# Kernel tuning notes

Measured on AMD Instinct MI355X. Metric: run time of the kernel, lower is better.

The kernel has to match this reference:

```python
import jax, jax.numpy as jnp
import numpy as np

N_GRAPHS = 512
NODES_PER_G = 200
EDGES_PER_G = 6400
N = N_GRAPHS * NODES_PER_G        # 102400 nodes
E = N_GRAPHS * EDGES_PER_G        # 3276800 edges
HID = 128
NCLS = 10


def _linear_params(key, fan_in, fan_out):
    # torch nn.Linear default init: U(-1/sqrt(fan_in), 1/sqrt(fan_in))
    s = 1.0 / np.sqrt(fan_in)
    kw, kb = jax.random.split(key)
    W = jax.random.uniform(kw, (fan_in, fan_out), minval=-s, maxval=s, dtype=jnp.float32)
    b = jax.random.uniform(kb, (fan_out,), minval=-s, maxval=s, dtype=jnp.float32)
    return W, b


def setup_inputs() -> dict:
    key = jax.random.key(0)
    ks = jax.random.split(key, 10)
    # edges are confined within each graph (DGL batched graph structure)
    g_off = (jnp.arange(E, dtype=jnp.int32) // EDGES_PER_G) * NODES_PER_G
    src = (g_off + jax.random.randint(ks[0], (E,), 0, NODES_PER_G)).astype(jnp.int32)
    dst = (g_off + jax.random.randint(ks[1], (E,), 0, NODES_PER_G)).astype(jnp.int32)
    W1, b1 = _linear_params(ks[2], 1, HID)
    W2, b2 = _linear_params(ks[3], HID, HID)
    Wa, ba = _linear_params(ks[4], HID, 512)
    Wb, bb = _linear_params(ks[5], 512, 1024)
    Wc, bc = _linear_params(ks[6], 1024, 1024)
    Wd, bd = _linear_params(ks[7], 1024, 512)
    We, be = _linear_params(ks[8], 512, NCLS)
    return dict(src=src, dst=dst, W1=W1, b1=b1, W2=W2, b2=b2,
                Wa=Wa, ba=ba, Wb=Wb, bb=bb, Wc=Wc, bc=bc,
                Wd=Wd, bd=bd, We=We, be=be)


def reference(src, dst, W1, b1, W2, b2, Wa, ba, Wb, bb, Wc, bc, Wd, bd, We, be):
    seg = jax.ops.segment_sum
    ones = jnp.ones((E,), jnp.float32)
    in_deg = seg(ones, dst, num_segments=N)    # [N]
    out_deg = seg(ones, src, num_segments=N)   # [N]
    # DGL GraphConv norm='both': degrees clamped to min 1
    inv_out = (1.0 / jnp.sqrt(jnp.maximum(out_deg, 1.0)))[:, None]
    inv_in = (1.0 / jnp.sqrt(jnp.maximum(in_deg, 1.0)))[:, None]

    def gconv(h, W, b):
        h = (h @ W) * inv_out                    # src-side normalize (weight applied first; same math)
        h = seg(h[src], dst, num_segments=N)     # gather + scatter-add aggregation
        return h * inv_in + b                    # dst-side normalize + bias

    h = in_deg[:, None]                          # input node features = in-degrees, [N,1]
    h = jax.nn.relu(gconv(h, W1, b1))
    h = jax.nn.relu(gconv(h, W2, b2))

    gid = jnp.arange(N, dtype=jnp.int32) // NODES_PER_G
    hg = seg(h, gid, num_segments=N_GRAPHS) / float(NODES_PER_G)  # mean readout, [G,HID]

    x = jax.nn.relu(hg @ Wa + ba)
    x = jax.nn.relu(x @ Wb + bb)
    x = jax.nn.relu(x @ Wc + bc)
    x = jax.nn.relu(x @ Wd + bd)
    return jax.nn.softmax(x @ We + be, axis=-1)  # nn.Softmax over class dim
```

## Files before the change

kernel.cpp:

```cpp
#include <hip/hip_runtime.h>
#include <stdint.h>

typedef unsigned short u16;
typedef unsigned int   u32;

#define NG   512
#define NPG  200
#define EPG  6400
#define NN   (NG*NPG)
#define NE_  (NG*EPG)
#define HID  128
#define KP   224
#define AW   224
#define AG   57344
#define ZP   136

__device__ __forceinline__ float bf2f(u16 b){ u32 u = ((u32)b) << 16; return __builtin_bit_cast(float, u); }
__device__ __forceinline__ u16 f2bf(float f){
    u32 u = __builtin_bit_cast(u32, f);
    u = (u + 0x7FFFu + ((u >> 16) & 1u)) >> 16;
    return (u16)u;
}

typedef __attribute__((ext_vector_type(8))) short bf16x8;
typedef __attribute__((ext_vector_type(4))) float f32x4;

enum : int { cW1=0, cb1=128, cb2=256, cba=384, cbb=896, cbc=1920, cbd=2944, cWe=3456, cbe=8576, cEND=8586 };
enum : int { T_Wa=0, T_Wb=65536, T_Wc=589824, T_Wd=1638400, T_END=2162688 };
enum : int { B0=8586, B1=24970, B2=2187658 };

struct PrepIn { const void* p[14]; };

__global__ __launch_bounds__(256) void k_prep(PrepIn in, float* __restrict__ canon,
                                              u16* __restrict__ W2T, u16* __restrict__ WTa)
{
    __shared__ int sflag;
    const int tid = threadIdx.x;
    if (tid < 64){
        const u16* wb = (const u16*)in.p[0];
        u16 a = wb[tid], b = wb[64 + tid];
        unsigned long long m1 = __ballot((int)((a >> 7) & 0xFF) >= 0x7F);
        unsigned long long m2 = __ballot((int)((b >> 7) & 0xFF) >= 0x7F);
        if (tid == 0) sflag = (__popcll(m1) + __popcll(m2) > 4) ? 1 : 0;
    }
    __syncthreads();
    const int f = sflag;

    int i = blockIdx.x * 256 + tid;
    if (i >= B2) return;

    if (i < B0){
        const void* s; int off;
        if      (i < 128) { s = in.p[0];  off = i; }
        else if (i < 256) { s = in.p[1];  off = i - 128; }
        else if (i < 384) { s = in.p[3];  off = i - 256; }
        else if (i < 896) { s = in.p[5];  off = i - 384; }
        else if (i < 1920){ s = in.p[7];  off = i - 896; }
        else if (i < 2944){ s = in.p[9];  off = i - 1920; }
        else if (i < 3456){ s = in.p[11]; off = i - 2944; }
        else if (i < 8576){ s = in.p[12]; off = i - 3456; }
        else              { s = in.p[13]; off = i - 8576; }
        canon[i] = f ? ((const float*)s)[off] : bf2f(((const u16*)s)[off]);
    } else if (i < B1){
        int j = i - B0;
        int outc = j >> 7, inc = j & 127;
        int si = inc * HID + outc;
        W2T[j] = f ? f2bf(((const float*)in.p[2])[si]) : ((const u16*)in.p[2])[si];
    } else {
        int j = i - B1;
        const void* s; int si;
        if (j < T_Wb){ s = in.p[4];  int n = j >> 7,  k = j & 127;  si = k*512  + n; }
        else if (j < T_Wc){ int jj = j - T_Wb; s = in.p[6];  int n = jj >> 9,  k = jj & 511;  si = k*1024 + n; }
        else if (j < T_Wd){ int jj = j - T_Wc; s = in.p[8];  int n = jj >> 10, k = jj & 1023; si = k*1024 + n; }
        else              { int jj = j - T_Wd; s = in.p[10]; int n = jj >> 10, k = jj & 1023; si = k*512  + n; }
        WTa[j] = f ? f2bf(((const float*)s)[si]) : ((const u16*)s)[si];
    }
}

__global__ __launch_bounds__(512) void k_graph_prep(
    const int* __restrict__ src, const int* __restrict__ dst,
    const float* __restrict__ W1, const float* __restrict__ b1,
    float* __restrict__ invInG, u16* __restrict__ h1sT,
    u16* __restrict__ Adense)
{
    __shared__ u32 A32[AG/2];
    __shared__ u16 srcL[EPG];
    __shared__ u16 dstL[EPG];
    __shared__ int degIn[NPG];
    __shared__ int degOut[NPG];
    __shared__ float sValL[NPG], sAgg[NPG], iiL[NPG], ioL[NPG], tL[NPG];
    __shared__ float w1L[HID], b1L[HID];

    const int g = blockIdx.x, tid = threadIdx.x;

    uint4* a4 = (uint4*)A32;
    #pragma unroll
    for (int i = 0; i < AG/8/512; i++)
        a4[i*512 + tid] = make_uint4(0,0,0,0);
    if (tid < NPG){ degIn[tid] = 0; degOut[tid] = 0; sAgg[tid] = 0.f; }
    if (tid < HID){ w1L[tid] = W1[tid]; b1L[tid] = b1[tid]; }
    __syncthreads();

    const int ebase = g * EPG;
    #pragma unroll
    for (int i = 0; i < (EPG + 511)/512; i++){
        int e = i*512 + tid;
        if (e < EPG){
            int s = src[ebase + e] - g*NPG;
            int d = dst[ebase + e] - g*NPG;
            srcL[e] = (u16)s; dstL[e] = (u16)d;
            atomicAdd(&degOut[s], 1);
            atomicAdd(&degIn[d], 1);
        }
    }
    __syncthreads();

    if (tid < NPG){
        int din = degIn[tid], dout = degOut[tid];
        float ii = rsqrtf(fmaxf((float)din, 1.f));
        float io = rsqrtf(fmaxf((float)dout, 1.f));
        iiL[tid] = ii; ioL[tid] = io;
        sValL[tid] = (float)din * io;
        invInG[g*NPG + tid] = ii;
    }
    __syncthreads();

    #pragma unroll
    for (int i = 0; i < (EPG + 511)/512; i++){
        int e = i*512 + tid;
        if (e < EPG){
            int s = srcL[e], d = dstL[e];
            int q = (d * 41) >> 11;
            int idx = (q*64 + (d - q*50))*AW + s;
            atomicAdd(&A32[idx >> 1], 1u << (16*(idx & 1)));
            atomicAdd(&sAgg[d], sValL[s]);
        }
    }
    __syncthreads();

    if (tid < NPG) tL[tid] = sAgg[tid] * iiL[tid];
    __syncthreads();

    const size_t base = (size_t)g * HID * KP;
    #pragma unroll 4
    for (int i = 0; i < HID*KP/512; i++){
        int idx = i*512 + tid;
        int c = idx / KP, v = idx - c*KP;
        u16 o = 0;
        if (v < NPG)
            o = f2bf(fmaxf(fmaf(tL[v], w1L[c], b1L[c]), 0.f) * ioL[v]);
        h1sT[base + idx] = o;
    }

    uint4* g4 = (uint4*)(Adense + (size_t)g * AG);
    #pragma unroll 4
    for (int i = 0; i < AG/8/512; i++){
        uint4 v = a4[i*512 + tid];
        u32* pv = (u32*)&v;
        #pragma unroll
        for (int j = 0; j < 4; j++){
            u32 wv = pv[j];
            pv[j] = (u32)f2bf((float)(wv & 0xFFFFu)) | ((u32)f2bf((float)(wv >> 16)) << 16);
        }
        g4[i*512 + tid] = v;
    }
}

__global__ __launch_bounds__(512, 4) void k_fused_graph(
    const u16* __restrict__ Adense,
    const u16* __restrict__ h1sT, const u16* __restrict__ W2T,
    const float* __restrict__ invInG, const float* __restrict__ b2,
    float* __restrict__ hg)
{
    __shared__ __align__(16) u16 Zs[256*ZP];
    __shared__ float invInL[256];
    __shared__ float b2L[HID];
    __shared__ float poolL[HID];

    const int g = blockIdx.x, tid = threadIdx.x;

    if (tid < HID){ b2L[tid] = b2[tid]; poolL[tid] = 0.f; }
    if (tid < 256){
        int dl = tid & 63;
        invInL[tid] = (dl < 50) ? invInG[g*NPG + (tid >> 6)*50 + dl] : 0.f;
    }

    const int w = tid >> 6, lane = tid & 63;
    const int wm = w >> 2, wn = w & 3;
    const int lr = lane & 15, quad = lane >> 4;

    const f32x4 fz = {0.f, 0.f, 0.f, 0.f};

    f32x4 acc[4][4];
    #pragma unroll
    for (int mi = 0; mi < 4; mi++)
        #pragma unroll
        for (int nt = 0; nt < 4; nt++) acc[mi][nt] = fz;
    {
        const u16* Ap = h1sT + (size_t)g * HID * KP + (size_t)(wm*64) * KP;
        const u16* Bp = Adense + (size_t)g * AG + (size_t)(wn*64) * AW;
        for (int ks = 0; ks < 7; ks++){
            bf16x8 af[4], bf[4];
            #pragma unroll
            for (int mi = 0; mi < 4; mi++)
                af[mi] = *(const bf16x8*)&Ap[(mi*16 + lr)*KP + ks*32 + quad*8];
            #pragma unroll
            for (int nt = 0; nt < 4; nt++)
                bf[nt] = *(const bf16x8*)&Bp[(nt*16 + lr)*AW + ks*32 + quad*8];
            #pragma unroll
            for (int mi = 0; mi < 4; mi++)
                #pragma unroll
                for (int nt = 0; nt < 4; nt++)
                    acc[mi][nt] = __builtin_amdgcn_mfma_f32_16x16x32_bf16(
                        af[mi], bf[nt], acc[mi][nt], 0, 0, 0);
        }
    }

    #pragma unroll
    for (int mi = 0; mi < 4; mi++)
        #pragma unroll
        for (int nt = 0; nt < 4; nt++){
            int vq = wn*64 + nt*16 + lr;
            int c0 = wm*64 + mi*16 + quad*4;
            u16 z0 = f2bf(acc[mi][nt][0]), z1 = f2bf(acc[mi][nt][1]);
            u16 z2 = f2bf(acc[mi][nt][2]), z3 = f2bf(acc[mi][nt][3]);
            uint2 pk = { (u32)z0 | ((u32)z1 << 16), (u32)z2 | ((u32)z3 << 16) };
            *(uint2*)&Zs[vq*ZP + c0] = pk;
        }
    __syncthreads();

    f32x4 acc2[2][8];
    #pragma unroll
    for (int mi = 0; mi < 2; mi++)
        #pragma unroll
        for (int nt = 0; nt < 8; nt++) acc2[mi][nt] = fz;
    for (int ks = 0; ks < 4; ks++){
        bf16x8 za[2];
        #pragma unroll
        for (int mi = 0; mi < 2; mi++)
            za[mi] = *(const bf16x8*)&Zs[((w + mi*8)*16 + lr)*ZP + ks*32 + quad*8];
        #pragma unroll
        for (int nt = 0; nt < 8; nt++){
            bf16x8 wb = *(const bf16x8*)&W2T[(size_t)(nt*16 + lr)*HID + ks*32 + quad*8];
            #pragma unroll
            for (int mi = 0; mi < 2; mi++)
                acc2[mi][nt] = __builtin_amdgcn_mfma_f32_16x16x32_bf16(
                    za[mi], wb, acc2[mi][nt], 0, 0, 0);
        }
    }

    #pragma unroll
    for (int mi = 0; mi < 2; mi++)
        #pragma unroll
        for (int nt = 0; nt < 8; nt++){
            int cout = nt*16 + lr;
            float s = 0.f;
            #pragma unroll
            for (int r = 0; r < 4; r++){
                int vq = (w + mi*8)*16 + quad*4 + r;
                if ((vq & 63) < 50)
                    s += fmaxf(fmaf(acc2[mi][nt][r], invInL[vq], b2L[cout]), 0.f);
            }
            atomicAdd(&poolL[cout], s);
        }
    __syncthreads();
    if (tid < HID) hg[(size_t)g*HID + tid] = poolL[tid] * (1.f / NPG);
}

template<int K, bool AF32>
__global__ __launch_bounds__(512) void k_mlp5(
    const void* __restrict__ Ahi_, const u16* __restrict__ Alo,
    const u16* __restrict__ WT, const float* __restrict__ bias,
    u16* __restrict__ Ohi, u16* __restrict__ Olo, int Nc)
{
    constexpr int ITERS = K / 64;
    __shared__ __align__(16) float red[32][68];

    const int tid = threadIdx.x;
    const int w = tid >> 6, lane = tid & 63;
    const int kz = w >> 2, wm = (w >> 1) & 1, wn = w & 1;
    const int lr = lane & 15, quad = lane >> 4;
    const int row0 = blockIdx.x * 32, col0 = blockIdx.y * 64;
    const int m = row0 + wm*16 + lr;
    const int k0 = kz * (K/2);

    const float* Af = (const float*)Ahi_;
    const u16*   Ah = (const u16*)Ahi_;

    auto loadA = [&](int it, bf16x8& hi, bf16x8& lo){
        const int kk = k0 + it*32 + quad*8;
        if constexpr (AF32){
            float xs[8];
            *(float4*)&xs[0] = *(const float4*)&Af[(size_t)m*K + kk];
            *(float4*)&xs[4] = *(const float4*)&Af[(size_t)m*K + kk + 4];
            #pragma unroll
            for (int j = 0; j < 8; j++){
                u16 hh = f2bf(xs[j]);
                hi[j] = (short)hh;
                lo[j] = (short)f2bf(xs[j] - bf2f(hh));
            }
        } else {
            hi = *(const bf16x8*)&Ah[(size_t)m*K + kk];
            lo = *(const bf16x8*)&Alo[(size_t)m*K + kk];
        }
    };
    auto loadB = [&](int it, bf16x8* b){
        const int kk = k0 + it*32 + quad*8;
        #pragma unroll
        for (int nt = 0; nt < 2; nt++){
            int n = col0 + wn*32 + nt*16 + lr;
            b[nt] = *(const bf16x8*)&WT[(size_t)n*K + kk];
        }
    };

    const f32x4 fz = {0.f, 0.f, 0.f, 0.f};
    f32x4 acc[2] = {fz, fz};
    bf16x8 chi, clo, cb[2], nhi, nlo, nb[2];
    loadA(0, chi, clo); loadB(0, cb);
    #pragma unroll 2
    for (int it = 0; it < ITERS; it++){
        if (it + 1 < ITERS){ loadA(it+1, nhi, nlo); loadB(it+1, nb); }
        #pragma unroll
        for (int nt = 0; nt < 2; nt++){
            acc[nt] = __builtin_amdgcn_mfma_f32_16x16x32_bf16(chi, cb[nt], acc[nt], 0, 0, 0);
            acc[nt] = __builtin_amdgcn_mfma_f32_16x16x32_bf16(clo, cb[nt], acc[nt], 0, 0, 0);
        }
        chi = nhi; clo = nlo; cb[0] = nb[0]; cb[1] = nb[1];
    }

    if (kz == 1){
        #pragma unroll
        for (int nt = 0; nt < 2; nt++)
            #pragma unroll
            for (int r = 0; r < 4; r++)
                red[wm*16 + quad*4 + r][wn*32 + nt*16 + lr] = acc[nt][r];
    }
    __syncthreads();
    if (kz == 0){
        #pragma unroll
        for (int nt = 0; nt < 2; nt++)
            #pragma unroll
            for (int r = 0; r < 4; r++){
                int rr = wm*16 + quad*4 + r;
                int cc = wn*32 + nt*16 + lr;
                float v = acc[nt][r] + red[rr][cc] + bias[col0 + cc];
                v = fmaxf(v, 0.f);
                u16 hh = f2bf(v);
                size_t go = (size_t)(row0 + rr) * Nc + col0 + cc;
                Ohi[go] = hh;
                Olo[go] = f2bf(v - bf2f(hh));
            }
    }
}

__global__ __launch_bounds__(64) void k_head(
    const u16* __restrict__ Xhi, const u16* __restrict__ Xlo,
    const float* __restrict__ We, const float* __restrict__ be,
    void* __restrict__ out, const u16* __restrict__ w1bits)
{
    const int g = blockIdx.x, lane = threadIdx.x;
    u16 a = w1bits[lane], b = w1bits[64 + lane];
    unsigned long long m1 = __ballot((int)((a >> 7) & 0xFF) >= 0x7F);
    unsigned long long m2 = __ballot((int)((b >> 7) & 0xFF) >= 0x7F);
    const int f = (__popcll(m1) + __popcll(m2) > 4) ? 1 : 0;

    float part[10];
    #pragma unroll
    for (int c = 0; c < 10; c++) part[c] = 0.f;
    for (int k = lane; k < 512; k += 64){
        float x = bf2f(Xhi[(size_t)g*512 + k]) + bf2f(Xlo[(size_t)g*512 + k]);
        #pragma unroll
        for (int c = 0; c < 10; c++) part[c] = fmaf(x, We[k*10 + c], part[c]);
    }
    #pragma unroll
    for (int c = 0; c < 10; c++){
        float v = part[c];
        for (int off = 32; off > 0; off >>= 1) v += __shfl_down(v, off);
        part[c] = v;
    }
    if (lane == 0){
        #pragma unroll
        for (int c = 0; c < 10; c++) part[c] += be[c];
        float m = part[0];
        #pragma unroll
        for (int c = 1; c < 10; c++) m = fmaxf(m, part[c]);
        float e[10], s = 0.f;
        #pragma unroll
        for (int c = 0; c < 10; c++){ e[c] = __expf(part[c] - m); s += e[c]; }
        float inv = 1.f / s;
        #pragma unroll
        for (int c = 0; c < 10; c++){
            float p = e[c] * inv;
            if (f) ((float*)out)[g*10 + c] = p;
            else   ((u16*)out)[g*10 + c]  = f2bf(p);
        }
    }
}

extern "C" void kernel_launch(void* const* d_in, const int* in_sizes, int n_in,
                              void* d_out, int out_size, void* d_ws, size_t ws_size,
                              hipStream_t stream)
{
    const int* src = (const int*)d_in[0];
    const int* dst = (const int*)d_in[1];

    char* ws = (char*)d_ws;
    size_t o = 0;
    float* canon    = (float*)(ws + o); o += ((size_t)cEND * 4 + 15) & ~(size_t)15;
    u16*   W2T      = (u16*)  (ws + o); o += (size_t)HID * HID * 2;
    u16*   WTa      = (u16*)  (ws + o); o += ((size_t)T_END * 2 + 15) & ~(size_t)15;
    float* invIn    = (float*)(ws + o); o += (size_t)NN * 4;
    u16*   Adense   = (u16*)  (ws + o); o += (size_t)NG * AG * 2;
    u16*   h1sT     = (u16*)  (ws + o); o += (size_t)NG * HID * KP * 2;
    float* hg       = (float*)(ws + o); o += (size_t)NG * HID * 4;
    u16*   X1hi     = (u16*)  (ws + o); o += (size_t)NG * 512 * 2;
    u16*   X1lo     = (u16*)  (ws + o); o += (size_t)NG * 512 * 2;
    u16*   X2hi     = (u16*)  (ws + o); o += (size_t)NG * 1024 * 2;
    u16*   X2lo     = (u16*)  (ws + o); o += (size_t)NG * 1024 * 2;
    u16*   X3hi     = (u16*)  (ws + o); o += (size_t)NG * 1024 * 2;
    u16*   X3lo     = (u16*)  (ws + o); o += (size_t)NG * 1024 * 2;
    u16*   X4hi     = (u16*)  (ws + o); o += (size_t)NG * 512 * 2;
    u16*   X4lo     = (u16*)  (ws + o); o += (size_t)NG * 512 * 2;
    (void)ws_size; (void)in_sizes; (void)n_in; (void)out_size;

    PrepIn pin;
    for (int i = 0; i < 14; i++) pin.p[i] = d_in[2 + i];
    k_prep<<<dim3((B2 + 255)/256), dim3(256), 0, stream>>>(pin, canon, W2T, WTa);

    const float *W1 = canon+cW1, *b1 = canon+cb1, *b2 = canon+cb2;
    const float *ba = canon+cba, *bb = canon+cbb, *bc = canon+cbc, *bd = canon+cbd;
    const float *We = canon+cWe, *be = canon+cbe;

    k_graph_prep<<<dim3(NG), dim3(512), 0, stream>>>(
        src, dst, W1, b1, invIn, h1sT, Adense);

    k_fused_graph<<<dim3(NG), dim3(512), 0, stream>>>(
        Adense, h1sT, W2T, invIn, b2, hg);

    k_mlp5<128,  true ><<<dim3(16, 8),  dim3(512), 0, stream>>>(hg,   nullptr, WTa + T_Wa, ba, X1hi, X1lo, 512);
    k_mlp5<512,  false><<<dim3(16, 16), dim3(512), 0, stream>>>(X1hi, X1lo,    WTa + T_Wb, bb, X2hi, X2lo, 1024);
    k_mlp5<1024, false><<<dim3(16, 16), dim3(512), 0, stream>>>(X2hi, X2lo,    WTa + T_Wc, bc, X3hi, X3lo, 1024);
    k_mlp5<1024, false><<<dim3(16, 8),  dim3(512), 0, stream>>>(X3hi, X3lo,    WTa + T_Wd, bd, X4hi, X4lo, 512);

    k_head<<<dim3(NG), dim3(64), 0, stream>>>(X4hi, X4lo, We, be, d_out, (const u16*)d_in[2]);
}
```

Measured before the change: 279.9 us.

## Fuse graph prep and GCN aggregation into one LDS-resident kernel, tile weight transposes

Merges the graph-preparation and fused-graph kernels into a single per-graph kernel. It keeps the edge list, h1 features and a quarter of the dense adjacency in shared memory and processes destination nodes in four 50-row chunks, so the dense adjacency and h1 intermediates are never written to or read back from global memory. The weight-prep kernel now transposes through a 64x64 shared-memory tile so both reads and writes are coalesced. The trade-off is heavier shared-memory use per block, which lowers occupancy, plus four extra passes over the edge list with more barriers.

```diff
diff --git a/kernel.cpp b/kernel.cpp
--- a/kernel.cpp
+++ b/kernel.cpp
@@ -10,9 +10,7 @@
 #define NN   (NG*NPG)
 #define NE_  (NG*EPG)
 #define HID  128
-#define KP   224
-#define AW   224
-#define AG   57344
+#define HS   232
 #define ZP   136
 
 __device__ __forceinline__ float bf2f(u16 b){ u32 u = ((u32)b) << 16; return __builtin_bit_cast(float, u); }
@@ -27,13 +25,13 @@
 
 enum : int { cW1=0, cb1=128, cb2=256, cba=384, cbb=896, cbc=1920, cbd=2944, cWe=3456, cbe=8576, cEND=8586 };
 enum : int { T_Wa=0, T_Wb=65536, T_Wc=589824, T_Wd=1638400, T_END=2162688 };
-enum : int { B0=8586, B1=24970, B2=2187658 };
 
 struct PrepIn { const void* p[14]; };
 
-__global__ __launch_bounds__(256) void k_prep(PrepIn in, float* __restrict__ canon,
-                                              u16* __restrict__ W2T, u16* __restrict__ WTa)
+__global__ __launch_bounds__(256) void k_prep2(PrepIn in, float* __restrict__ canon,
+                                               u16* __restrict__ W2T, u16* __restrict__ WTa)
 {
+    __shared__ u16 tile[64][72];
     __shared__ int sflag;
     const int tid = threadIdx.x;
     if (tid < 64){
@@ -45,60 +43,67 @@
     }
     __syncthreads();
     const int f = sflag;
-
-    int i = blockIdx.x * 256 + tid;
-    if (i >= B2) return;
-
-    if (i < B0){
-        const void* s; int off;
-        if      (i < 128) { s = in.p[0];  off = i; }
-        else if (i < 256) { s = in.p[1];  off = i - 128; }
-        else if (i < 384) { s = in.p[3];  off = i - 256; }
-        else if (i < 896) { s = in.p[5];  off = i - 384; }
-        else if (i < 1920){ s = in.p[7];  off = i - 896; }
-        else if (i < 2944){ s = in.p[9];  off = i - 1920; }
-        else if (i < 3456){ s = in.p[11]; off = i - 2944; }
-        else if (i < 8576){ s = in.p[12]; off = i - 3456; }
-        else              { s = in.p[13]; off = i - 8576; }
-        canon[i] = f ? ((const float*)s)[off] : bf2f(((const u16*)s)[off]);
-    } else if (i < B1){
-        int j = i - B0;
-        int outc = j >> 7, inc = j & 127;
-        int si = inc * HID + outc;
-        W2T[j] = f ? f2bf(((const float*)in.p[2])[si]) : ((const u16*)in.p[2])[si];
+    const int bid = blockIdx.x;
+
+    if (bid < 532){
+        const void* s; u16* dst; int K, N, t, lgn;
+        if      (bid < 4)  { t = bid;       s = in.p[2];  dst = W2T;        K = 128;  N = 128;  lgn = 1; }
+        else if (bid < 20) { t = bid - 4;   s = in.p[4];  dst = WTa + T_Wa; K = 128;  N = 512;  lgn = 3; }
+        else if (bid < 148){ t = bid - 20;  s = in.p[6];  dst = WTa + T_Wb; K = 512;  N = 1024; lgn = 4; }
+        else if (bid < 404){ t = bid - 148; s = in.p[8];  dst = WTa + T_Wc; K = 1024; N = 1024; lgn = 4; }
+        else               { t = bid - 404; s = in.p[10]; dst = WTa + T_Wd; K = 1024; N = 512;  lgn = 3; }
+        const int k0 = (t >> lgn) * 64, n0 = (t & ((1 << lgn) - 1)) * 64;
+        #pragma unroll
+        for (int i = 0; i < 16; i++){
+            int idx = i*256 + tid;
+            int kk = idx >> 6, nn = idx & 63;
+            int si = (k0 + kk)*N + n0 + nn;
+            tile[nn][kk] = f ? f2bf(((const float*)s)[si]) : ((const u16*)s)[si];
+        }
+        __syncthreads();
+        #pragma unroll
+        for (int i = 0; i < 16; i++){
+            int idx = i*256 + tid;
+            int nn = idx >> 6, kk = idx & 63;
+            dst[(size_t)(n0 + nn)*K + k0 + kk] = tile[nn][kk];
+        }
     } else {
-        int j = i - B1;
-        const void* s; int si;
-        if (j < T_Wb){ s = in.p[4];  int n = j >> 7,  k = j & 127;  si = k*512  + n; }
-        else if (j < T_Wc){ int jj = j - T_Wb; s = in.p[6];  int n = jj >> 9,  k = jj & 511;  si = k*1024 + n; }
-        else if (j < T_Wd){ int jj = j - T_Wc; s = in.p[8];  int n = jj >> 10, k = jj & 1023; si = k*1024 + n; }
-        else              { int jj = j - T_Wd; s = in.p[10]; int n = jj >> 10, k = jj & 1023; si = k*512  + n; }
-        WTa[j] = f ? f2bf(((const float*)s)[si]) : ((const u16*)s)[si];
-    }
-}
-
-__global__ __launch_bounds__(512) void k_graph_prep(
+        int i = (bid - 532)*256 + tid;
+        if (i < cEND){
+            const void* s; int off;
+            if      (i < 128) { s = in.p[0];  off = i; }
+            else if (i < 256) { s = in.p[1];  off = i - 128; }
+            else if (i < 384) { s = in.p[3];  off = i - 256; }
+            else if (i < 896) { s = in.p[5];  off = i - 384; }
+            else if (i < 1920){ s = in.p[7];  off = i - 896; }
+            else if (i < 2944){ s = in.p[9];  off = i - 1920; }
+            else if (i < 3456){ s = in.p[11]; off = i - 2944; }
+            else if (i < 8576){ s = in.p[12]; off = i - 3456; }
+            else              { s = in.p[13]; off = i - 8576; }
+            canon[i] = f ? ((const float*)s)[off] : bf2f(((const u16*)s)[off]);
+        }
+    }
+}
+
+__global__ __launch_bounds__(512) void k_mega(
     const int* __restrict__ src, const int* __restrict__ dst,
     const float* __restrict__ W1, const float* __restrict__ b1,
-    float* __restrict__ invInG, u16* __restrict__ h1sT,
-    u16* __restrict__ Adense)
+    const float* __restrict__ b2, const u16* __restrict__ W2T,
+    float* __restrict__ hg)
 {
-    __shared__ u32 A32[AG/2];
-    __shared__ u16 srcL[EPG];
-    __shared__ u16 dstL[EPG];
-    __shared__ int degIn[NPG];
-    __shared__ int degOut[NPG];
-    __shared__ float sValL[NPG], sAgg[NPG], iiL[NPG], ioL[NPG], tL[NPG];
-    __shared__ float w1L[HID], b1L[HID];
+    __shared__ u32 pkE[EPG];
+    __shared__ __align__(16) u16 h1s[HID*HS];
+    __shared__ __align__(16) u16 Aq[64*HS];
+    __shared__ __align__(16) u16 Zq[64*ZP];
+    __shared__ int degIn[NPG], degOut[NPG];
+    __shared__ float sVal[NPG], sAgg[NPG], iiL[NPG], ioL[NPG], tL[NPG];
+    __shared__ float w1L[HID], b1L[HID], b2L[HID], poolL[HID];
 
     const int g = blockIdx.x, tid = threadIdx.x;
-
-    uint4* a4 = (uint4*)A32;
-    #pragma unroll
-    for (int i = 0; i < AG/8/512; i++)
-        a4[i*512 + tid] = make_uint4(0,0,0,0);
+    u32* aq32 = (u32*)Aq;
+
     if (tid < NPG){ degIn[tid] = 0; degOut[tid] = 0; sAgg[tid] = 0.f; }
-    if (tid < HID){ w1L[tid] = W1[tid]; b1L[tid] = b1[tid]; }
+    if (tid < HID){ w1L[tid] = W1[tid]; b1L[tid] = b1[tid]; b2L[tid] = b2[tid]; poolL[tid] = 0.f; }
     __syncthreads();
 
     const int ebase = g * EPG;
@@ -108,7 +113,7 @@
         if (e < EPG){
             int s = src[ebase + e] - g*NPG;
             int d = dst[ebase + e] - g*NPG;
-            srcL[e] = (u16)s; dstL[e] = (u16)d;
+            pkE[e] = (u32)s | ((u32)d << 16);
             atomicAdd(&degOut[s], 1);
             atomicAdd(&degIn[d], 1);
         }
@@ -116,12 +121,10 @@
     __syncthreads();
 
     if (tid < NPG){
-        int din = degIn[tid], dout = degOut[tid];
-        float ii = rsqrtf(fmaxf((float)din, 1.f));
-        float io = rsqrtf(fmaxf((float)dout, 1.f));
+        float ii = rsqrtf(fmaxf((float)degIn[tid], 1.f));
+        float io = rsqrtf(fmaxf((float)degOut[tid], 1.f));
         iiL[tid] = ii; ioL[tid] = io;
-        sValL[tid] = (float)din * io;
-        invInG[g*NPG + tid] = ii;
+        sVal[tid] = (float)degIn[tid] * io;
     }
     __syncthreads();
 
@@ -129,141 +132,126 @@
     for (int i = 0; i < (EPG + 511)/512; i++){
         int e = i*512 + tid;
         if (e < EPG){
-            int s = srcL[e], d = dstL[e];
-            int q = (d * 41) >> 11;
-            int idx = (q*64 + (d - q*50))*AW + s;
-            atomicAdd(&A32[idx >> 1], 1u << (16*(idx & 1)));
-            atomicAdd(&sAgg[d], sValL[s]);
-        }
-    }
-    __syncthreads();
-
+            u32 u = pkE[e];
+            atomicAdd(&sAgg[u >> 16], sVal[u & 0xFFFF]);
+        }
+    }
+    __syncthreads();
     if (tid < NPG) tL[tid] = sAgg[tid] * iiL[tid];
     __syncthreads();
 
-    const size_t base = (size_t)g * HID * KP;
     #pragma unroll 4
-    for (int i = 0; i < HID*KP/512; i++){
+    for (int i = 0; i < HID*HS/512; i++){
         int idx = i*512 + tid;
-        int c = idx / KP, v = idx - c*KP;
+        int c = idx / HS, v = idx - c*HS;
         u16 o = 0;
         if (v < NPG)
             o = f2bf(fmaxf(fmaf(tL[v], w1L[c], b1L[c]), 0.f) * ioL[v]);
-        h1sT[base + idx] = o;
-    }
-
-    uint4* g4 = (uint4*)(Adense + (size_t)g * AG);
-    #pragma unroll 4
-    for (int i = 0; i < AG/8/512; i++){
-        uint4 v = a4[i*512 + tid];
-        u32* pv = (u32*)&v;
-        #pragma unroll
-        for (int j = 0; j < 4; j++){
-            u32 wv = pv[j];
-            pv[j] = (u32)f2bf((float)(wv & 0xFFFFu)) | ((u32)f2bf((float)(wv >> 16)) << 16);
-        }
-        g4[i*512 + tid] = v;
-    }
-}
-
-__global__ __launch_bounds__(512, 4) void k_fused_graph(
-    const u16* __restrict__ Adense,
-    const u16* __restrict__ h1sT, const u16* __restrict__ W2T,
-    const float* __restrict__ invInG, const float* __restrict__ b2,
-    float* __restrict__ hg)
-{
-    __shared__ __align__(16) u16 Zs[256*ZP];
-    __shared__ float invInL[256];
-    __shared__ float b2L[HID];
-    __shared__ float poolL[HID];
-
-    const int g = blockIdx.x, tid = threadIdx.x;
-
-    if (tid < HID){ b2L[tid] = b2[tid]; poolL[tid] = 0.f; }
-    if (tid < 256){
-        int dl = tid & 63;
-        invInL[tid] = (dl < 50) ? invInG[g*NPG + (tid >> 6)*50 + dl] : 0.f;
-    }
+        h1s[idx] = o;
+    }
+    __syncthreads();
 
     const int w = tid >> 6, lane = tid & 63;
-    const int wm = w >> 2, wn = w & 3;
     const int lr = lane & 15, quad = lane >> 4;
-
     const f32x4 fz = {0.f, 0.f, 0.f, 0.f};
 
-    f32x4 acc[4][4];
-    #pragma unroll
-    for (int mi = 0; mi < 4; mi++)
-        #pragma unroll
-        for (int nt = 0; nt < 4; nt++) acc[mi][nt] = fz;
-    {
-        const u16* Ap = h1sT + (size_t)g * HID * KP + (size_t)(wm*64) * KP;
-        const u16* Bp = Adense + (size_t)g * AG + (size_t)(wn*64) * AW;
+    for (int q = 0; q < 4; q++){
+        uint4* a4 = (uint4*)Aq;
+        for (int i = tid; i < 64*HS/8; i += 512) a4[i] = make_uint4(0,0,0,0);
+        __syncthreads();
+        #pragma unroll
+        for (int i = 0; i < (EPG + 511)/512; i++){
+            int e = i*512 + tid;
+            if (e < EPG){
+                u32 u = pkE[e];
+                int s = u & 0xFFFF, d = u >> 16;
+                int qe = (d * 41) >> 11;
+                if (qe == q){
+                    int idx = (d - q*50)*HS + s;
+                    atomicAdd(&aq32[idx >> 1], 1u << (16*(idx & 1)));
+                }
+            }
+        }
+        __syncthreads();
+        for (int i = tid; i < 64*HS/2; i += 512){
+            u32 wv = aq32[i];
+            if (wv)
+                aq32[i] = (u32)f2bf((float)(wv & 0xFFFFu)) | ((u32)f2bf((float)(wv >> 16)) << 16);
+        }
+        __syncthreads();
+
+        const int wm = w >> 1, wn = w & 1;
+        f32x4 acc[2][2];
+        #pragma unroll
+        for (int mi = 0; mi < 2; mi++)
+            #pragma unroll
+            for (int nt = 0; nt < 2; nt++) acc[mi][nt] = fz;
         for (int ks = 0; ks < 7; ks++){
-            bf16x8 af[4], bf[4];
-            #pragma unroll
-            for (int mi = 0; mi < 4; mi++)
-                af[mi] = *(const bf16x8*)&Ap[(mi*16 + lr)*KP + ks*32 + quad*8];
-            #pragma unroll
-            for (int nt = 0; nt < 4; nt++)
-                bf[nt] = *(const bf16x8*)&Bp[(nt*16 + lr)*AW + ks*32 + quad*8];
-            #pragma unroll
-            for (int mi = 0; mi < 4; mi++)
+            bf16x8 af[2], bf[2];
+            #pragma unroll
+            for (int mi = 0; mi < 2; mi++)
+                af[mi] = *(const bf16x8*)&h1s[(wm*32 + mi*16 + lr)*HS + ks*32 + quad*8];
+            #pragma unroll
+            for (int nt = 0; nt < 2; nt++)
+                bf[nt] = *(const bf16x8*)&Aq[(wn*32 + nt*16 + lr)*HS + ks*32 + quad*8];
+            #pragma unroll
+            for (int mi = 0; mi < 2; mi++)
                 #pragma unroll
-                for (int nt = 0; nt < 4; nt++)
+                for (int nt = 0; nt < 2; nt++)
                     acc[mi][nt] = __builtin_amdgcn_mfma_f32_16x16x32_bf16(
                         af[mi], bf[nt], acc[mi][nt], 0, 0, 0);
         }
-    }
-
-    #pragma unroll
-    for (int mi = 0; mi < 4; mi++)
-        #pragma unroll
-        for (int nt = 0; nt < 4; nt++){
-            int vq = wn*64 + nt*16 + lr;
-            int c0 = wm*64 + mi*16 + quad*4;
-            u16 z0 = f2bf(acc[mi][nt][0]), z1 = f2bf(acc[mi][nt][1]);
-            u16 z2 = f2bf(acc[mi][nt][2]), z3 = f2bf(acc[mi][nt][3]);
-            uint2 pk = { (u32)z0 | ((u32)z1 << 16), (u32)z2 | ((u32)z3 << 16) };
-            *(uint2*)&Zs[vq*ZP + c0] = pk;
-        }
-    __syncthreads();
-
-    f32x4 acc2[2][8];
-    #pragma unroll
-    for (int mi = 0; mi < 2; mi++)
-        #pragma unroll
-        for (int nt = 0; nt < 8; nt++) acc2[mi][nt] = fz;
-    for (int ks = 0; ks < 4; ks++){
-        bf16x8 za[2];
         #pragma unroll
         for (int mi = 0; mi < 2; mi++)
-            za[mi] = *(const bf16x8*)&Zs[((w + mi*8)*16 + lr)*ZP + ks*32 + quad*8];
-        #pragma unroll
-        for (int nt = 0; nt < 8; nt++){
-            bf16x8 wb = *(const bf16x8*)&W2T[(size_t)(nt*16 + lr)*HID + ks*32 + quad*8];
+            #pragma unroll
+            for (int nt = 0; nt < 2; nt++){
+                int vq = wn*32 + nt*16 + lr;
+                int c0 = wm*32 + mi*16 + quad*4;
+                u16 z0 = f2bf(acc[mi][nt][0]), z1 = f2bf(acc[mi][nt][1]);
+                u16 z2 = f2bf(acc[mi][nt][2]), z3 = f2bf(acc[mi][nt][3]);
+                uint2 pk = { (u32)z0 | ((u32)z1 << 16), (u32)z2 | ((u32)z3 << 16) };
+                *(uint2*)&Zq[vq*ZP + c0] = pk;
+            }
+        __syncthreads();
+
+        const int wm2 = w >> 2, wn2 = w & 3;
+        f32x4 acc2[2][2];
+        #pragma unroll
+        for (int mi = 0; mi < 2; mi++)
+            #pragma unroll
+            for (int nt = 0; nt < 2; nt++) acc2[mi][nt] = fz;
+        for (int ks = 0; ks < 4; ks++){
+            bf16x8 za[2], wb[2];
             #pragma unroll
             for (int mi = 0; mi < 2; mi++)
-                acc2[mi][nt] = __builtin_amdgcn_mfma_f32_16x16x32_bf16(
-                    za[mi], wb, acc2[mi][nt], 0, 0, 0);
-        }
-    }
-
-    #pragma unroll
-    for (int mi = 0; mi < 2; mi++)
-        #pragma unroll
-        for (int nt = 0; nt < 8; nt++){
-            int cout = nt*16 + lr;
-            float s = 0.f;
-            #pragma unroll
-            for (int r = 0; r < 4; r++){
-                int vq = (w + mi*8)*16 + quad*4 + r;
-                if ((vq & 63) < 50)
-                    s += fmaxf(fmaf(acc2[mi][nt][r], invInL[vq], b2L[cout]), 0.f);
+                za[mi] = *(const bf16x8*)&Zq[(wm2*32 + mi*16 + lr)*ZP + ks*32 + quad*8];
+            #pragma unroll
+            for (int nt = 0; nt < 2; nt++)
+                wb[nt] = *(const bf16x8*)&W2T[(size_t)(wn2*32 + nt*16 + lr)*HID + ks*32 + quad*8];
+            #pragma unroll
+            for (int mi = 0; mi < 2; mi++)
+                #pragma unroll
+                for (int nt = 0; nt < 2; nt++)
+                    acc2[mi][nt] = __builtin_amdgcn_mfma_f32_16x16x32_bf16(
+                        za[mi], wb[nt], acc2[mi][nt], 0, 0, 0);
+        }
+        #pragma unroll
+        for (int mi = 0; mi < 2; mi++)
+            #pragma unroll
+            for (int nt = 0; nt < 2; nt++){
+                int cout = wn2*32 + nt*16 + lr;
+                float s = 0.f;
+                #pragma unroll
+                for (int r = 0; r < 4; r++){
+                    int vq = wm2*32 + mi*16 + quad*4 + r;
+                    if (vq < 50)
+                        s += fmaxf(fmaf(acc2[mi][nt][r], iiL[q*50 + vq], b2L[cout]), 0.f);
+                }
+                atomicAdd(&poolL[cout], s);
             }
-            atomicAdd(&poolL[cout], s);
-        }
-    __syncthreads();
+        __syncthreads();
+    }
+
     if (tid < HID) hg[(size_t)g*HID + tid] = poolL[tid] * (1.f / NPG);
 }
 
@@ -409,9 +397,6 @@
     float* canon    = (float*)(ws + o); o += ((size_t)cEND * 4 + 15) & ~(size_t)15;
     u16*   W2T      = (u16*)  (ws + o); o += (size_t)HID * HID * 2;
     u16*   WTa      = (u16*)  (ws + o); o += ((size_t)T_END * 2 + 15) & ~(size_t)15;
-    float* invIn    = (float*)(ws + o); o += (size_t)NN * 4;
-    u16*   Adense   = (u16*)  (ws + o); o += (size_t)NG * AG * 2;
-    u16*   h1sT     = (u16*)  (ws + o); o += (size_t)NG * HID * KP * 2;
     float* hg       = (float*)(ws + o); o += (size_t)NG * HID * 4;
     u16*   X1hi     = (u16*)  (ws + o); o += (size_t)NG * 512 * 2;
     u16*   X1lo     = (u16*)  (ws + o); o += (size_t)NG * 512 * 2;
@@ -425,17 +410,13 @@
 
     PrepIn pin;
     for (int i = 0; i < 14; i++) pin.p[i] = d_in[2 + i];
-    k_prep<<<dim3((B2 + 255)/256), dim3(256), 0, stream>>>(pin, canon, W2T, WTa);
+    k_prep2<<<dim3(566), dim3(256), 0, stream>>>(pin, canon, W2T, WTa);
 
     const float *W1 = canon+cW1, *b1 = canon+cb1, *b2 = canon+cb2;
     const float *ba = canon+cba, *bb = canon+cbb, *bc = canon+cbc, *bd = canon+cbd;
     const float *We = canon+cWe, *be = canon+cbe;
 
-    k_graph_prep<<<dim3(NG), dim3(512), 0, stream>>>(
-        src, dst, W1, b1, invIn, h1sT, Adense);
-
-    k_fused_graph<<<dim3(NG), dim3(512), 0, stream>>>(
-        Adense, h1sT, W2T, invIn, b2, hg);
+    k_mega<<<dim3(NG), dim3(512), 0, stream>>>(src, dst, W1, b1, b2, W2T, hg);
 
     k_mlp5<128,  true ><<<dim3(16, 8),  dim3(512), 0, stream>>>(hg,   nullptr, WTa + T_Wa, ba, X1hi, X1lo, 512);
     k_mlp5<512,  false><<<dim3(16, 16), dim3(512), 0, stream>>>(X1hi, X1lo,    WTa + T_Wb, bb, X2hi, X2lo, 1024);
```

Measured after the change: 255.7 us. 8.7% less time.
